# Kernel tuning notes

Measured on AMD Instinct MI355X. Metric: run time of the kernel, lower is better.

## Reference

```python
import jax, jax.numpy as jnp
import numpy as np

IN_F = 4096
OUT_F = 4096
B, S = 2, 2048


def setup_inputs() -> dict:
    key = jax.random.key(0)
    k1, k2, k3, k4 = jax.random.split(key, 4)
    input = jax.random.normal(k1, (B, S, IN_F), dtype=jnp.float32)
    int8_weights = jax.random.randint(k2, (OUT_F, IN_F), -128, 128, dtype=jnp.int32).astype(jnp.int8)
    scales = jax.random.normal(k3, (OUT_F,), dtype=jnp.float32)
    bias = jax.random.normal(k4, (1, OUT_F), dtype=jnp.float32)
    return {"input": input, "int8_weights": int8_weights, "scales": scales, "bias": bias}


def reference(input, int8_weights, scales, bias):
    # F.linear(x, W) = x @ W.T ; dequant via per-output-channel scale, then bias
    w = int8_weights.astype(input.dtype)          # [out, in]
    out = jnp.einsum('bsi,oi->bso', input, w)     # [B, S, out]
    out = out * scales + bias                      # broadcast [out] and [1, out]
    return out
```

## Files before the change

### kernel.cpp

```cpp
#include <hip/hip_runtime.h>
#include <hip/hip_bf16.h>

typedef unsigned short u16;
typedef unsigned int u32;
typedef unsigned char u8;
typedef __attribute__((ext_vector_type(4))) int i32x4;

#define MM 4096
#define NN 4096
#define KK 4096

#define BAR __builtin_amdgcn_s_barrier()
#define FENCE asm volatile("" ::: "memory")
#define WAITVM(n) asm volatile("s_waitcnt vmcnt(" #n ")" ::: "memory")

#define ABUF(sh, b) ((sh) + (b) * 32768)
#define BBUF(sh, b) ((sh) + 16384 + (b) * 32768)

__global__ __launch_bounds__(256) void cvt_w_k(const int* __restrict__ w,
                                               u8* __restrict__ o) {
  int i = blockIdx.x * 256 + threadIdx.x;
  const int4* w4 = (const int4*)w + (size_t)i * 4;
  i32x4 r;
#pragma unroll
  for (int j = 0; j < 4; ++j) {
    int4 v = w4[j];
    r[j] = (v.x & 255) | ((v.y & 255) << 8) | ((v.z & 255) << 16) | ((u32)(v.w & 255) << 24);
  }
  *(i32x4*)(o + (size_t)i * 16) = r;
}

__global__ __launch_bounds__(256) void cvt_a_k(const float* __restrict__ x,
                                               u8* __restrict__ o,
                                               float* __restrict__ dA) {
  const int row = blockIdx.x;
  const float4* xr = (const float4*)(x + (size_t)row * KK);
  const int t = threadIdx.x;
  float4 v[4];
  float mx = 0.f;
#pragma unroll
  for (int j = 0; j < 4; ++j) {
    v[j] = xr[t + j * 256];
    mx = fmaxf(mx, fmaxf(fmaxf(fabsf(v[j].x), fabsf(v[j].y)),
                         fmaxf(fabsf(v[j].z), fabsf(v[j].w))));
  }
#pragma unroll
  for (int off = 32; off; off >>= 1) mx = fmaxf(mx, __shfl_down(mx, off));
  __shared__ float sm[4];
  if ((t & 63) == 0) sm[t >> 6] = mx;
  __syncthreads();
  mx = fmaxf(fmaxf(sm[0], sm[1]), fmaxf(sm[2], sm[3]));
  mx = fmaxf(mx, 1e-20f);
  const float inv = 127.0f / mx;
  if (t == 0) dA[row] = mx / 127.0f;
  u32* orow = (u32*)(o + (size_t)row * KK);
#pragma unroll
  for (int j = 0; j < 4; ++j) {
    int qx = (int)rintf(v[j].x * inv), qy = (int)rintf(v[j].y * inv);
    int qz = (int)rintf(v[j].z * inv), qw = (int)rintf(v[j].w * inv);
    orow[t + j * 256] =
        (qx & 255) | ((qy & 255) << 8) | ((qz & 255) << 16) | ((u32)(qw & 255) << 24);
  }
}

__device__ __forceinline__ void gload16(const u8* g, u8* l) {
  __builtin_amdgcn_global_load_lds(
      (const __attribute__((address_space(1))) void*)g,
      (__attribute__((address_space(3))) void*)l, 16, 0, 0);
}

__device__ __forceinline__ void stage_half(const u8* __restrict__ gRowBase,
                                           int k0, u8* ldsHalf, int tid) {
  int row = tid >> 2;
  int c = (tid & 3) ^ ((row >> 1) & 3);
  gload16(gRowBase + (size_t)row * KK + k0 + c * 16, ldsHalf + tid * 16);
}

__device__ __forceinline__ i32x4 ldsfrag(const u8* base, int r, int q) {
  return *(const i32x4*)(base + r * 64 + (((q ^ (r >> 1)) & 3) << 4));
}

#define MFMAI8(a, b, c) __builtin_amdgcn_mfma_i32_16x16x64_i8(a, b, c, 0, 0, 0)

template <int MODE>
__device__ __forceinline__ void do_tile(
    int t, i32x4 (&acc)[8][4], const u8* Ag, const u8* Wg, u8* sh,
    int tid, int lr, int hi, int wr, int wc) {
  const int b = t & 1;
  u8* Acur = ABUF(sh, b);
  u8* Anxt = ABUF(sh, b ^ 1);
  u8* Bcur = BBUF(sh, b);
  i32x4 bfr[4], afr[4];

#pragma unroll
  for (int n = 0; n < 2; ++n)
    bfr[n] = ldsfrag(Bcur, wc * 64 + n * 16 + lr, hi);
#pragma unroll
  for (int m = 0; m < 4; ++m)
    afr[m] = ldsfrag(Acur, wr * 128 + m * 16 + lr, hi);
  if (MODE <= 1) stage_half(Ag + 128 * KK, (t + 1) * 64, Anxt + 8192, tid);
  FENCE; BAR;
  __builtin_amdgcn_s_setprio(1);
#pragma unroll
  for (int m = 0; m < 4; ++m)
#pragma unroll
    for (int n = 0; n < 2; ++n)
      acc[m][n] = MFMAI8(afr[m], bfr[n], acc[m][n]);
  __builtin_amdgcn_s_setprio(0);
  FENCE; BAR;

#pragma unroll
  for (int n = 2; n < 4; ++n)
    bfr[n] = ldsfrag(Bcur, wc * 64 + n * 16 + lr, hi);
  FENCE; BAR;
  __builtin_amdgcn_s_setprio(1);
#pragma unroll
  for (int m = 0; m < 4; ++m)
#pragma unroll
    for (int n = 0; n < 2; ++n)
      acc[m][2 + n] = MFMAI8(afr[m], bfr[2 + n], acc[m][2 + n]);
  __builtin_amdgcn_s_setprio(0);
  FENCE; BAR;

#pragma unroll
  for (int m = 0; m < 4; ++m)
    afr[m] = ldsfrag(Acur, wr * 128 + 64 + m * 16 + lr, hi);
  if (MODE == 0) stage_half(Wg, (t + 2) * 64, Bcur, tid);
  FENCE; BAR;
  __builtin_amdgcn_s_setprio(1);
#pragma unroll
  for (int m = 0; m < 4; ++m)
#pragma unroll
    for (int n = 0; n < 2; ++n)
      acc[4 + m][n] = MFMAI8(afr[m], bfr[n], acc[4 + m][n]);
  __builtin_amdgcn_s_setprio(0);
  FENCE; BAR;

  if (MODE == 0) {
    stage_half(Wg + 128 * KK, (t + 2) * 64, Bcur + 8192, tid);
    stage_half(Ag, (t + 2) * 64, Acur, tid);
    WAITVM(3);
  } else if (MODE == 1) {
    WAITVM(0);
  }
  FENCE; BAR;
  __builtin_amdgcn_s_setprio(1);
#pragma unroll
  for (int m = 0; m < 4; ++m)
#pragma unroll
    for (int n = 0; n < 2; ++n)
      acc[4 + m][2 + n] = MFMAI8(afr[m], bfr[2 + n], acc[4 + m][2 + n]);
  __builtin_amdgcn_s_setprio(0);
  FENCE; BAR;
}

__global__ __launch_bounds__(512, 2) void gemm_k(const u8* __restrict__ A,
                                                 const u8* __restrict__ W,
                                                 const float* __restrict__ dA,
                                                 const float* __restrict__ scales,
                                                 const float* __restrict__ bias,
                                                 float* __restrict__ out) {
  __shared__ u8 sh[65536];

  const int cpx = gridDim.x >> 3;
  const int wg = (blockIdx.x & 7) * cpx + (blockIdx.x >> 3);
  const int bm = wg >> 4;
  const int bn = wg & 15;

  const int tid = threadIdx.x;
  const int lane = tid & 63;
  const int lr = lane & 15;
  const int hi = lane >> 4;
  const int wid = tid >> 6;
  const int wr = wid >> 2;
  const int wc = wid & 3;

  i32x4 acc[8][4] = {};

  const u8* Ag = A + (size_t)bm * 256 * KK;
  const u8* Wg = W + (size_t)bn * 256 * KK;

  stage_half(Wg,             0, BBUF(sh, 0),        tid);
  stage_half(Wg + 128 * KK,  0, BBUF(sh, 0) + 8192, tid);
  stage_half(Ag,             0, ABUF(sh, 0),        tid);
  stage_half(Ag + 128 * KK,  0, ABUF(sh, 0) + 8192, tid);
  stage_half(Wg,            64, BBUF(sh, 1),        tid);
  stage_half(Wg + 128 * KK, 64, BBUF(sh, 1) + 8192, tid);
  stage_half(Ag,            64, ABUF(sh, 1),        tid);
  WAITVM(3);
  BAR;

  for (int t = 0; t < 62; ++t)
    do_tile<0>(t, acc, Ag, Wg, sh, tid, lr, hi, wr, wc);
  do_tile<1>(62, acc, Ag, Wg, sh, tid, lr, hi, wr, wc);
  do_tile<2>(63, acc, Ag, Wg, sh, tid, lr, hi, wr, wc);

  const int colb = bn * 256 + wc * 64 + lr;
  const int rowb0 = bm * 256 + wr * 128 + (hi << 2);
#pragma unroll
  for (int m = 0; m < 8; ++m) {
    const int row = rowb0 + m * 16;
    const float da0 = dA[row], da1 = dA[row + 1], da2 = dA[row + 2], da3 = dA[row + 3];
#pragma unroll
    for (int n = 0; n < 4; ++n) {
      const int col = colb + n * 16;
      const float sc = scales[col];
      const float bi = bias[col];
      out[(size_t)(row + 0) * NN + col] = (float)acc[m][n][0] * (da0 * sc) + bi;
      out[(size_t)(row + 1) * NN + col] = (float)acc[m][n][1] * (da1 * sc) + bi;
      out[(size_t)(row + 2) * NN + col] = (float)acc[m][n][2] * (da2 * sc) + bi;
      out[(size_t)(row + 3) * NN + col] = (float)acc[m][n][3] * (da3 * sc) + bi;
    }
  }
}

__global__ __launch_bounds__(256) void fb_k(const float* __restrict__ A,
                                            const int* __restrict__ W,
                                            const float* __restrict__ scales,
                                            const float* __restrict__ bias,
                                            float* __restrict__ out) {
  __shared__ float Arow[KK];
  const int m = blockIdx.y;
  const int n0 = blockIdx.x * 256;
  const int tid = threadIdx.x;
  for (int k = tid; k < KK; k += 256) Arow[k] = A[(size_t)m * KK + k];
  __syncthreads();
  const int n = n0 + tid;
  float acc = 0.f;
  const int* wrp = W + (size_t)n * KK;
  for (int k = 0; k < KK; ++k) acc += Arow[k] * (float)wrp[k];
  out[(size_t)m * NN + n] = acc * scales[n] + bias[n];
}

extern "C" void kernel_launch(void* const* d_in, const int* in_sizes, int n_in,
                              void* d_out, int out_size, void* d_ws, size_t ws_size,
                              hipStream_t stream) {
  const float* input = (const float*)d_in[0];
  const int* w8 = (const int*)d_in[1];
  const float* scales = (const float*)d_in[2];
  const float* bias = (const float*)d_in[3];
  float* out = (float*)d_out;

  const size_t nelem = (size_t)NN * KK;
  const size_t need = 2 * nelem + MM * sizeof(float);

  if (ws_size >= need) {
    u8* Wq = (u8*)d_ws;
    u8* Aq = Wq + nelem;
    float* dA = (float*)(Aq + nelem);
    cvt_w_k<<<4096, 256, 0, stream>>>(w8, Wq);
    cvt_a_k<<<MM, 256, 0, stream>>>(input, Aq, dA);
    gemm_k<<<256, 512, 0, stream>>>(Aq, Wq, dA, scales, bias, out);
  } else {
    dim3 grid(NN / 256, MM);
    fb_k<<<grid, 256, 0, stream>>>(input, w8, scales, bias, out);
  }
}
```

Measured before the change: 98.69 us.

## Software-pipeline LDS fragment loads across MFMA phases, prefetching next tile's fragments

Restructures the per-tile schedule so that LDS fragment reads for the next phase (and the first A/B fragments of the next K tile) are issued while the current MFMA group runs. Fragment registers now persist across tiles, and the barrier count per tile drops from eight to four. Global staging is reordered so that both W halves are issued together, then both A halves, with adjusted vmcnt waits. The cost is extra live fragment registers, which pressures the two-workgroups-per-CU occupancy target, plus tighter reasoning about LDS buffer reuse hazards.

```diff
diff --git a/kernel.cpp b/kernel.cpp
--- a/kernel.cpp
+++ b/kernel.cpp
@@ -85,71 +85,72 @@
 template <int MODE>
 __device__ __forceinline__ void do_tile(
     int t, i32x4 (&acc)[8][4], const u8* Ag, const u8* Wg, u8* sh,
-    int tid, int lr, int hi, int wr, int wc) {
+    int tid, int lr, int hi, int wr, int wc,
+    i32x4 (&afr0)[4], i32x4 (&afr1)[4], i32x4 (&bfr01)[2], i32x4 (&bfr23)[2]) {
   const int b = t & 1;
   u8* Acur = ABUF(sh, b);
   u8* Anxt = ABUF(sh, b ^ 1);
   u8* Bcur = BBUF(sh, b);
-  i32x4 bfr[4], afr[4];
+  u8* Bnxt = BBUF(sh, b ^ 1);
 
 #pragma unroll
   for (int n = 0; n < 2; ++n)
-    bfr[n] = ldsfrag(Bcur, wc * 64 + n * 16 + lr, hi);
-#pragma unroll
-  for (int m = 0; m < 4; ++m)
-    afr[m] = ldsfrag(Acur, wr * 128 + m * 16 + lr, hi);
-  if (MODE <= 1) stage_half(Ag + 128 * KK, (t + 1) * 64, Anxt + 8192, tid);
-  FENCE; BAR;
-  __builtin_amdgcn_s_setprio(1);
-#pragma unroll
-  for (int m = 0; m < 4; ++m)
-#pragma unroll
-    for (int n = 0; n < 2; ++n)
-      acc[m][n] = MFMAI8(afr[m], bfr[n], acc[m][n]);
-  __builtin_amdgcn_s_setprio(0);
-  FENCE; BAR;
-
-#pragma unroll
-  for (int n = 2; n < 4; ++n)
-    bfr[n] = ldsfrag(Bcur, wc * 64 + n * 16 + lr, hi);
-  FENCE; BAR;
-  __builtin_amdgcn_s_setprio(1);
-#pragma unroll
-  for (int m = 0; m < 4; ++m)
-#pragma unroll
-    for (int n = 0; n < 2; ++n)
-      acc[m][2 + n] = MFMAI8(afr[m], bfr[2 + n], acc[m][2 + n]);
-  __builtin_amdgcn_s_setprio(0);
-  FENCE; BAR;
-
-#pragma unroll
-  for (int m = 0; m < 4; ++m)
-    afr[m] = ldsfrag(Acur, wr * 128 + 64 + m * 16 + lr, hi);
-  if (MODE == 0) stage_half(Wg, (t + 2) * 64, Bcur, tid);
-  FENCE; BAR;
-  __builtin_amdgcn_s_setprio(1);
-#pragma unroll
-  for (int m = 0; m < 4; ++m)
-#pragma unroll
-    for (int n = 0; n < 2; ++n)
-      acc[4 + m][n] = MFMAI8(afr[m], bfr[n], acc[4 + m][n]);
-  __builtin_amdgcn_s_setprio(0);
-  FENCE; BAR;
-
+    bfr23[n] = ldsfrag(Bcur, wc * 64 + (2 + n) * 16 + lr, hi);
+  __builtin_amdgcn_s_setprio(1);
+#pragma unroll
+  for (int m = 0; m < 4; ++m)
+#pragma unroll
+    for (int n = 0; n < 2; ++n)
+      acc[m][n] = MFMAI8(afr0[m], bfr01[n], acc[m][n]);
+  __builtin_amdgcn_s_setprio(0);
+  FENCE; BAR;
+
+#pragma unroll
+  for (int m = 0; m < 4; ++m)
+    afr1[m] = ldsfrag(Acur, wr * 128 + 64 + m * 16 + lr, hi);
   if (MODE == 0) {
+    stage_half(Wg,            (t + 2) * 64, Bcur,        tid);
     stage_half(Wg + 128 * KK, (t + 2) * 64, Bcur + 8192, tid);
-    stage_half(Ag, (t + 2) * 64, Acur, tid);
-    WAITVM(3);
-  } else if (MODE == 1) {
-    WAITVM(0);
-  }
-  FENCE; BAR;
-  __builtin_amdgcn_s_setprio(1);
-#pragma unroll
-  for (int m = 0; m < 4; ++m)
-#pragma unroll
-    for (int n = 0; n < 2; ++n)
-      acc[4 + m][2 + n] = MFMAI8(afr[m], bfr[2 + n], acc[4 + m][2 + n]);
+  }
+  __builtin_amdgcn_s_setprio(1);
+#pragma unroll
+  for (int m = 0; m < 4; ++m)
+#pragma unroll
+    for (int n = 0; n < 2; ++n)
+      acc[m][2 + n] = MFMAI8(afr0[m], bfr23[n], acc[m][2 + n]);
+  __builtin_amdgcn_s_setprio(0);
+  if (MODE == 0) { WAITVM(2); } else if (MODE == 1) { WAITVM(0); }
+  FENCE; BAR;
+
+  if (MODE <= 1) {
+#pragma unroll
+    for (int m = 0; m < 4; ++m)
+      afr0[m] = ldsfrag(Anxt, wr * 128 + m * 16 + lr, hi);
+  }
+  if (MODE == 0) {
+    stage_half(Ag,            (t + 2) * 64, Acur,        tid);
+    stage_half(Ag + 128 * KK, (t + 2) * 64, Acur + 8192, tid);
+  }
+  __builtin_amdgcn_s_setprio(1);
+#pragma unroll
+  for (int m = 0; m < 4; ++m)
+#pragma unroll
+    for (int n = 0; n < 2; ++n)
+      acc[4 + m][n] = MFMAI8(afr1[m], bfr01[n], acc[4 + m][n]);
+  __builtin_amdgcn_s_setprio(0);
+  FENCE; BAR;
+
+  if (MODE <= 1) {
+#pragma unroll
+    for (int n = 0; n < 2; ++n)
+      bfr01[n] = ldsfrag(Bnxt, wc * 64 + n * 16 + lr, hi);
+  }
+  __builtin_amdgcn_s_setprio(1);
+#pragma unroll
+  for (int m = 0; m < 4; ++m)
+#pragma unroll
+    for (int n = 0; n < 2; ++n)
+      acc[4 + m][2 + n] = MFMAI8(afr1[m], bfr23[n], acc[4 + m][2 + n]);
   __builtin_amdgcn_s_setprio(0);
   FENCE; BAR;
 }
@@ -176,6 +177,7 @@
   const int wc = wid & 3;
 
   i32x4 acc[8][4] = {};
+  i32x4 afr0[4], afr1[4], bfr01[2], bfr23[2];
 
   const u8* Ag = A + (size_t)bm * 256 * KK;
   const u8* Wg = W + (size_t)bn * 256 * KK;
@@ -187,13 +189,20 @@
   stage_half(Wg,            64, BBUF(sh, 1),        tid);
   stage_half(Wg + 128 * KK, 64, BBUF(sh, 1) + 8192, tid);
   stage_half(Ag,            64, ABUF(sh, 1),        tid);
-  WAITVM(3);
+  stage_half(Ag + 128 * KK, 64, ABUF(sh, 1) + 8192, tid);
+  WAITVM(4);
   BAR;
+#pragma unroll
+  for (int m = 0; m < 4; ++m)
+    afr0[m] = ldsfrag(ABUF(sh, 0), wr * 128 + m * 16 + lr, hi);
+#pragma unroll
+  for (int n = 0; n < 2; ++n)
+    bfr01[n] = ldsfrag(BBUF(sh, 0), wc * 64 + n * 16 + lr, hi);
 
   for (int t = 0; t < 62; ++t)
-    do_tile<0>(t, acc, Ag, Wg, sh, tid, lr, hi, wr, wc);
-  do_tile<1>(62, acc, Ag, Wg, sh, tid, lr, hi, wr, wc);
-  do_tile<2>(63, acc, Ag, Wg, sh, tid, lr, hi, wr, wc);
+    do_tile<0>(t, acc, Ag, Wg, sh, tid, lr, hi, wr, wc, afr0, afr1, bfr01, bfr23);
+  do_tile<1>(62, acc, Ag, Wg, sh, tid, lr, hi, wr, wc, afr0, afr1, bfr01, bfr23);
+  do_tile<2>(63, acc, Ag, Wg, sh, tid, lr, hi, wr, wc, afr0, afr1, bfr01, bfr23);
 
   const int colb = bn * 256 + wc * 64 + lr;
   const int rowb0 = bm * 256 + wr * 128 + (hi << 2);
```

New measurement: 97.49 us. No clear change (-1.2%).
